# Kernel tuning notes

Hardware: AMD Instinct MI355X
Metric: run time of the kernel (lower is better)

Reference implementation:

```python
import jax, jax.numpy as jnp
import numpy as np

B = 131072
# join branch layer dims: 203 -> 175 -> 150 -> 128 -> 80 -> 48
DIMS = [203, 175, 150, 128, 80, 48]

def setup_inputs() -> dict:
    key = jax.random.key(0)
    ks = jax.random.split(key, 11)
    inp = {"x": jax.random.normal(ks[0], (B, DIMS[0]), dtype=jnp.float32)}
    for i in range(5):
        fan_in, fan_out = DIMS[i], DIMS[i + 1]
        bound = 1.0 / np.sqrt(fan_in)
        inp[f"W{i+1}"] = jax.random.uniform(ks[1 + 2 * i], (fan_out, fan_in), minval=-bound, maxval=bound, dtype=jnp.float32)
        inp[f"b{i+1}"] = jax.random.uniform(ks[2 + 2 * i], (fan_out,), minval=-bound, maxval=bound, dtype=jnp.float32)
    return inp

def reference(x, W1, b1, W2, b2, W3, b3, W4, b4, W5, b5):
    # join branch of NodeEmbedding, dropout in eval mode (identity).
    h = jnp.tanh(x @ W1.T + b1)      # [B,175]
    h = jnp.tanh(h @ W2.T + b2)      # [B,150]
    h = jnp.tanh(h @ W3.T + b3)      # [B,128]
    h = jnp.tanh(h @ W4.T + b4)      # [B,80]
    return h @ W5.T + b5             # [B,48], no activation on last layer
```

## Files before the change

kernel.cpp:

```cpp
#include <hip/hip_runtime.h>


typedef short short8 __attribute__((ext_vector_type(8)));
typedef float f32x16 __attribute__((ext_vector_type(16)));
typedef unsigned int uint;
typedef unsigned short ushort;

#define SROW 196
#define WBHALF 12288


__device__ __forceinline__ ushort f2bf(float f) {
    uint u = __float_as_uint(f);
    u += 0x7FFFu + ((u >> 16) & 1u);
    return (ushort)(u >> 16);
}
__device__ __forceinline__ float bf2f(ushort h) { return __uint_as_float(((uint)h) << 16); }
__device__ __forceinline__ float fast_tanh(float x) {
    float e = __expf(2.0f * x);
    return 1.0f - 2.0f / (e + 1.0f);
}
__device__ __forceinline__ void g2l16(const void* g, void* l) {
    __builtin_amdgcn_global_load_lds((const __attribute__((address_space(1))) uint*)g,
                                     (__attribute__((address_space(3))) uint*)l, 16, 0, 0);
}

union U16x8 { uint u[4]; short8 s; };

__device__ __forceinline__ short8 load_a_lds(const ushort* p) {
    U16x8 r;
    *(uint2*)&r.u[0] = *(const uint2*)(p);
    *(uint2*)&r.u[2] = *(const uint2*)(p + 4);
    return r.s;
}

__global__ void prep_weights(const float* __restrict__ W1, const float* __restrict__ W2,
                             const float* __restrict__ W3, const float* __restrict__ W4,
                             const float* __restrict__ W5, char* __restrict__ ws)
{
    const int b = blockIdx.x, l = threadIdx.x;
    int layer, local;
    if      (b <  78) { layer = 0; local = b; }
    else if (b < 133) { layer = 1; local = b - 78; }
    else if (b < 173) { layer = 2; local = b - 133; }
    else if (b < 197) { layer = 3; local = b - 173; }
    else              { layer = 4; local = b - 197; }
    const int NTa[5]  = {6, 5, 4, 3, 2};
    const int FINa[5] = {203, 175, 150, 128, 80};
    const int FOa[5]  = {175, 150, 128, 80, 48};
    const float* Wp = (layer == 0) ? W1 : (layer == 1) ? W2 : (layer == 2) ? W3
                    : (layer == 3) ? W4 : W5;
    const int nt = NTa[layer], fin = FINa[layer], fout = FOa[layer];
    const int c = local / nt, t = local % nt;
    const int n  = t * 32 + (l & 31);
    const int kb = c * 16 + (l >> 5) * 8;
    uint hw[4], lw[4];
#pragma unroll
    for (int j = 0; j < 8; ++j) {
        int k = kb + j;
        float v = (n < fout && k < fin) ? Wp[(size_t)n * fin + k] : 0.0f;
        ushort hh = f2bf(v);
        ushort ll = f2bf(v - bf2f(hh));
        if (j & 1) { hw[j >> 1] |= ((uint)hh) << 16; lw[j >> 1] |= ((uint)ll) << 16; }
        else       { hw[j >> 1]  = hh;               lw[j >> 1]  = ll; }
    }
    char* dst = ws + (size_t)b * 2048 + l * 16;
    *(uint4*)dst          = make_uint4(hw[0], hw[1], hw[2], hw[3]);
    *(uint4*)(dst + 1024) = make_uint4(lw[0], lw[1], lw[2], lw[3]);
}

template<int KC, int NT, bool ACT, bool LAST, bool FIRST>
__device__ __forceinline__ void run_layer(
    const char* __restrict__ wsL, const float* __restrict__ bias, int FOUT,
    const float* __restrict__ xg,
    const ushort* __restrict__ aHp, const ushort* __restrict__ aLp,
    ushort* __restrict__ oHp, ushort* __restrict__ oLp,
    float* __restrict__ outg,
    char* __restrict__ wbuf, int row0, int tid)
{
    const int l  = tid & 63;
    const int w  = tid >> 6;
    const int rg = w >> 1;
    const int ns = w & 1;
    const int lx = l & 31;
    const int lh = l >> 5;
    constexpr int MT = (NT + 1) / 2;

    f32x16 acc[MT];
#pragma unroll
    for (int m = 0; m < MT; ++m) {
        int t = ns + 2 * m;
        float bv = 0.0f;
        if (t < NT) { int n = t * 32 + lx; bv = (n < FOUT) ? bias[n] : 0.0f; }
#pragma unroll
        for (int r = 0; r < 16; ++r) acc[m][r] = bv;
    }

    __syncthreads();
    for (int idx = w; idx < 2 * NT; idx += 4)
        g2l16(wsL + (size_t)((idx >> 1)) * 2048 + (idx & 1) * 1024 + l * 16,
              wbuf + idx * 1024);

#pragma unroll 1
    for (int c = 0; c < KC; ++c) {
        __syncthreads();
        if (c + 1 < KC) {
            char* dst = wbuf + ((c + 1) & 1) * WBHALF;
            for (int idx = w; idx < 2 * NT; idx += 4)
                g2l16(wsL + (size_t)((c + 1) * NT + (idx >> 1)) * 2048 + (idx & 1) * 1024 + l * 16,
                      dst + idx * 1024);
        }
        short8 aH, aL;
        if (FIRST) {
            float v[8];
#pragma unroll
            for (int j = 0; j < 8; ++j) {
                int k = c * 16 + lh * 8 + j;
                v[j] = (k < 203) ? xg[(size_t)(rg * 32 + lx) * 203 + k] : 0.0f;
            }
            U16x8 h, lo;
#pragma unroll
            for (int j = 0; j < 8; ++j) {
                ushort hh = f2bf(v[j]);
                ushort ll = f2bf(v[j] - bf2f(hh));
                if (j & 1) { h.u[j >> 1] |= ((uint)hh) << 16; lo.u[j >> 1] |= ((uint)ll) << 16; }
                else       { h.u[j >> 1]  = hh;               lo.u[j >> 1]  = ll; }
            }
            aH = h.s; aL = lo.s;
        } else {
            const int off = (rg * 32 + lx) * SROW + c * 16 + lh * 8;
            aH = load_a_lds(aHp + off);
            aL = load_a_lds(aLp + off);
        }
        const char* cb = wbuf + (c & 1) * WBHALF;
#pragma unroll
        for (int m = 0; m < MT; ++m) {
            int t = ns + 2 * m;
            if (t < NT) {
                short8 bH = *(const short8*)(cb + (2 * t) * 1024 + l * 16);
                short8 bL = *(const short8*)(cb + (2 * t + 1) * 1024 + l * 16);
                acc[m] = __builtin_amdgcn_mfma_f32_32x32x16_bf16(aH, bH, acc[m], 0, 0, 0);
                acc[m] = __builtin_amdgcn_mfma_f32_32x32x16_bf16(aL, bH, acc[m], 0, 0, 0);
                acc[m] = __builtin_amdgcn_mfma_f32_32x32x16_bf16(aH, bL, acc[m], 0, 0, 0);
            }
        }
    }
    __syncthreads();

#pragma unroll
    for (int m = 0; m < MT; ++m) {
        int t = ns + 2 * m;
        if (t < NT) {
#pragma unroll
            for (int r = 0; r < 16; ++r) {
                float vv = acc[m][r];
                if (ACT) vv = fast_tanh(vv);
                int rowl = rg * 32 + (r & 3) + 8 * (r >> 2) + 4 * lh;
                int col  = t * 32 + lx;
                if (LAST) {
                    if (col < 48)
                        outg[(size_t)(row0 + rowl) * 48 + col] = vv;
                } else {
                    ushort hh = f2bf(vv);
                    ushort ll = f2bf(vv - bf2f(hh));
                    oHp[rowl * SROW + col] = hh;
                    oLp[rowl * SROW + col] = ll;
                }
            }
        }
    }
}

__global__ __launch_bounds__(256, 2)
void mlp_mfma(const float* __restrict__ x,
              const float* __restrict__ b1, const float* __restrict__ b2,
              const float* __restrict__ b3, const float* __restrict__ b4,
              const float* __restrict__ b5,
              const char* __restrict__ ws, float* __restrict__ out)
{
    __shared__ __align__(16) ushort actH[64 * SROW];
    __shared__ __align__(16) ushort actL[64 * SROW];
    __shared__ __align__(16) char   wbuf[2 * WBHALF];

    const int tid  = threadIdx.x;
    const int row0 = blockIdx.x * 64;
    const float* xg = x + (size_t)row0 * 203;

    run_layer<13, 6, true,  false, true >(ws,              b1, 175, xg,      nullptr, nullptr, actH, actL, nullptr, wbuf, row0, tid);
    run_layer<11, 5, true,  false, false>(ws +  78 * 2048, b2, 150, nullptr, actH, actL, actH, actL, nullptr, wbuf, row0, tid);
    run_layer<10, 4, true,  false, false>(ws + 133 * 2048, b3, 128, nullptr, actH, actL, actH, actL, nullptr, wbuf, row0, tid);
    run_layer< 8, 3, true,  false, false>(ws + 173 * 2048, b4,  80, nullptr, actH, actL, actH, actL, nullptr, wbuf, row0, tid);
    run_layer< 5, 2, false, true,  false>(ws + 197 * 2048, b5,  48, nullptr, actH, actL, actH, actL, out,     wbuf, row0, tid);
}

extern "C" void kernel_launch(void* const* d_in, const int* in_sizes, int n_in,
                              void* d_out, int out_size, void* d_ws, size_t ws_size,
                              hipStream_t stream) {
    (void)in_sizes; (void)n_in; (void)ws_size; (void)out_size;
    const float* x  = (const float*)d_in[0];
    const float* W1 = (const float*)d_in[1];
    const float* b1 = (const float*)d_in[2];
    const float* W2 = (const float*)d_in[3];
    const float* b2 = (const float*)d_in[4];
    const float* W3 = (const float*)d_in[5];
    const float* b3 = (const float*)d_in[6];
    const float* W4 = (const float*)d_in[7];
    const float* b4 = (const float*)d_in[8];
    const float* W5 = (const float*)d_in[9];
    const float* b5 = (const float*)d_in[10];
    float* out = (float*)d_out;
    char* ws = (char*)d_ws;

    hipLaunchKernelGGL(prep_weights, dim3(207), dim3(64), 0, stream,
                       W1, W2, W3, W4, W5, ws);
    hipLaunchKernelGGL(mlp_mfma, dim3(131072 / 64), dim3(256), 0, stream,
                       x, b1, b2, b3, b4, b5, ws, out);
}
```

Before: 344.3 us.

## Read weights directly from global, pack hi/lo activations, stage x coalesced via LDS

```diff
diff --git a/kernel.cpp b/kernel.cpp
--- a/kernel.cpp
+++ b/kernel.cpp
@@ -6,9 +6,8 @@
 typedef unsigned int uint;
 typedef unsigned short ushort;
 
-#define SROW 196
-#define WBHALF 12288
-
+#define SROW 180
+#define XSTR 20
 
 __device__ __forceinline__ ushort f2bf(float f) {
     uint u = __float_as_uint(f);
@@ -20,19 +19,12 @@
     float e = __expf(2.0f * x);
     return 1.0f - 2.0f / (e + 1.0f);
 }
-__device__ __forceinline__ void g2l16(const void* g, void* l) {
-    __builtin_amdgcn_global_load_lds((const __attribute__((address_space(1))) uint*)g,
-                                     (__attribute__((address_space(3))) uint*)l, 16, 0, 0);
-}
-
-union U16x8 { uint u[4]; short8 s; };
-
-__device__ __forceinline__ short8 load_a_lds(const ushort* p) {
-    U16x8 r;
-    *(uint2*)&r.u[0] = *(const uint2*)(p);
-    *(uint2*)&r.u[2] = *(const uint2*)(p + 4);
-    return r.s;
-}
+__device__ __forceinline__ uint rbf(float v) {
+    uint u = __float_as_uint(v);
+    return u + 0x7FFFu + ((u >> 16) & 1u);
+}
+
+union U4S8 { uint4 u; short8 s; };
 
 __global__ void prep_weights(const float* __restrict__ W1, const float* __restrict__ W2,
                              const float* __restrict__ W3, const float* __restrict__ W4,
@@ -69,84 +61,10 @@
     *(uint4*)(dst + 1024) = make_uint4(lw[0], lw[1], lw[2], lw[3]);
 }
 
-template<int KC, int NT, bool ACT, bool LAST, bool FIRST>
-__device__ __forceinline__ void run_layer(
-    const char* __restrict__ wsL, const float* __restrict__ bias, int FOUT,
-    const float* __restrict__ xg,
-    const ushort* __restrict__ aHp, const ushort* __restrict__ aLp,
-    ushort* __restrict__ oHp, ushort* __restrict__ oLp,
-    float* __restrict__ outg,
-    char* __restrict__ wbuf, int row0, int tid)
-{
-    const int l  = tid & 63;
-    const int w  = tid >> 6;
-    const int rg = w >> 1;
-    const int ns = w & 1;
-    const int lx = l & 31;
-    const int lh = l >> 5;
-    constexpr int MT = (NT + 1) / 2;
-
-    f32x16 acc[MT];
-#pragma unroll
-    for (int m = 0; m < MT; ++m) {
-        int t = ns + 2 * m;
-        float bv = 0.0f;
-        if (t < NT) { int n = t * 32 + lx; bv = (n < FOUT) ? bias[n] : 0.0f; }
-#pragma unroll
-        for (int r = 0; r < 16; ++r) acc[m][r] = bv;
-    }
-
-    __syncthreads();
-    for (int idx = w; idx < 2 * NT; idx += 4)
-        g2l16(wsL + (size_t)((idx >> 1)) * 2048 + (idx & 1) * 1024 + l * 16,
-              wbuf + idx * 1024);
-
-#pragma unroll 1
-    for (int c = 0; c < KC; ++c) {
-        __syncthreads();
-        if (c + 1 < KC) {
-            char* dst = wbuf + ((c + 1) & 1) * WBHALF;
-            for (int idx = w; idx < 2 * NT; idx += 4)
-                g2l16(wsL + (size_t)((c + 1) * NT + (idx >> 1)) * 2048 + (idx & 1) * 1024 + l * 16,
-                      dst + idx * 1024);
-        }
-        short8 aH, aL;
-        if (FIRST) {
-            float v[8];
-#pragma unroll
-            for (int j = 0; j < 8; ++j) {
-                int k = c * 16 + lh * 8 + j;
-                v[j] = (k < 203) ? xg[(size_t)(rg * 32 + lx) * 203 + k] : 0.0f;
-            }
-            U16x8 h, lo;
-#pragma unroll
-            for (int j = 0; j < 8; ++j) {
-                ushort hh = f2bf(v[j]);
-                ushort ll = f2bf(v[j] - bf2f(hh));
-                if (j & 1) { h.u[j >> 1] |= ((uint)hh) << 16; lo.u[j >> 1] |= ((uint)ll) << 16; }
-                else       { h.u[j >> 1]  = hh;               lo.u[j >> 1]  = ll; }
-            }
-            aH = h.s; aL = lo.s;
-        } else {
-            const int off = (rg * 32 + lx) * SROW + c * 16 + lh * 8;
-            aH = load_a_lds(aHp + off);
-            aL = load_a_lds(aLp + off);
-        }
-        const char* cb = wbuf + (c & 1) * WBHALF;
-#pragma unroll
-        for (int m = 0; m < MT; ++m) {
-            int t = ns + 2 * m;
-            if (t < NT) {
-                short8 bH = *(const short8*)(cb + (2 * t) * 1024 + l * 16);
-                short8 bL = *(const short8*)(cb + (2 * t + 1) * 1024 + l * 16);
-                acc[m] = __builtin_amdgcn_mfma_f32_32x32x16_bf16(aH, bH, acc[m], 0, 0, 0);
-                acc[m] = __builtin_amdgcn_mfma_f32_32x32x16_bf16(aL, bH, acc[m], 0, 0, 0);
-                acc[m] = __builtin_amdgcn_mfma_f32_32x32x16_bf16(aH, bL, acc[m], 0, 0, 0);
-            }
-        }
-    }
-    __syncthreads();
-
+template<int MT, int NT, int FOUT, int PADN, bool ACT, bool LAST>
+__device__ __forceinline__ void d_phase(f32x16* acc, uint* oP, float* outg,
+                                        int row0, int rg, int ns, int lx, int lh, int tid)
+{
 #pragma unroll
     for (int m = 0; m < MT; ++m) {
         int t = ns + 2 * m;
@@ -158,39 +76,177 @@
                 int rowl = rg * 32 + (r & 3) + 8 * (r >> 2) + 4 * lh;
                 int col  = t * 32 + lx;
                 if (LAST) {
-                    if (col < 48)
-                        outg[(size_t)(row0 + rowl) * 48 + col] = vv;
-                } else {
-                    ushort hh = f2bf(vv);
-                    ushort ll = f2bf(vv - bf2f(hh));
-                    oHp[rowl * SROW + col] = hh;
-                    oLp[rowl * SROW + col] = ll;
+                    if (col < 48) outg[(size_t)(row0 + rowl) * 48 + col] = vv;
+                } else if (col < FOUT) {
+                    uint r1  = rbf(vv);
+                    uint hib = r1 & 0xFFFF0000u;
+                    float lo = vv - __uint_as_float(hib);
+                    uint r2  = rbf(lo);
+                    oP[rowl * SROW + col] = hib | (r2 >> 16);
                 }
             }
         }
     }
-}
-
-__global__ __launch_bounds__(256, 2)
+    if (!LAST) {
+        if (PADN > 0) {
+            for (int idx = tid; idx < 64 * PADN; idx += 256) {
+                int row = idx / PADN, p = idx % PADN;
+                oP[row * SROW + FOUT + p] = 0u;
+            }
+        }
+        __syncthreads();
+    }
+}
+
+template<int KC, int NT, int FOUT, int PADN, bool ACT, bool LAST>
+__device__ __forceinline__ void run_layer(const char* __restrict__ wsL,
+    const float* __restrict__ bias, const uint* aP, uint* oP, float* outg,
+    int row0, int l, int rg, int ns, int lx, int lh, int tid)
+{
+    constexpr int MT = (NT + 1) / 2;
+    f32x16 acc[MT];
+#pragma unroll
+    for (int m = 0; m < MT; ++m) {
+        int t = ns + 2 * m;
+        float bv = 0.0f;
+        if (t < NT) { int n = t * 32 + lx; bv = (n < FOUT) ? bias[n] : 0.0f; }
+#pragma unroll
+        for (int r = 0; r < 16; ++r) acc[m][r] = bv;
+    }
+
+#pragma unroll
+    for (int c = 0; c < KC; ++c) {
+        U4S8 bh[MT], bl[MT];
+#pragma unroll
+        for (int m = 0; m < MT; ++m) {
+            int t = ns + 2 * m;
+            if (t < NT) {
+                const uint4* w = (const uint4*)wsL + (size_t)((c * NT + t) * 2) * 64 + l;
+                bh[m].u = w[0];
+                bl[m].u = w[64];
+            }
+        }
+        const uint* ap = aP + (rg * 32 + lx) * SROW + c * 16 + lh * 8;
+        uint4 d0 = *(const uint4*)ap;
+        uint4 d1 = *(const uint4*)(ap + 4);
+        uint dd[8] = {d0.x, d0.y, d0.z, d0.w, d1.x, d1.y, d1.z, d1.w};
+        U4S8 ah, al;
+        uint* aHu = (uint*)&ah; uint* aLu = (uint*)&al;
+#pragma unroll
+        for (int j = 0; j < 4; ++j) {
+            aHu[j] = (dd[2*j] >> 16)     | (dd[2*j + 1] & 0xFFFF0000u);
+            aLu[j] = (dd[2*j] & 0xFFFFu) | (dd[2*j + 1] << 16);
+        }
+#pragma unroll
+        for (int m = 0; m < MT; ++m) {
+            int t = ns + 2 * m;
+            if (t < NT) {
+                acc[m] = __builtin_amdgcn_mfma_f32_32x32x16_bf16(ah.s, bh[m].s, acc[m], 0, 0, 0);
+                acc[m] = __builtin_amdgcn_mfma_f32_32x32x16_bf16(al.s, bh[m].s, acc[m], 0, 0, 0);
+                acc[m] = __builtin_amdgcn_mfma_f32_32x32x16_bf16(ah.s, bl[m].s, acc[m], 0, 0, 0);
+            }
+        }
+    }
+    if (!LAST) __syncthreads();
+    d_phase<MT, NT, FOUT, PADN, ACT, LAST>(acc, oP, outg, row0, rg, ns, lx, lh, tid);
+}
+
+__device__ __forceinline__ void run_first(const float* __restrict__ x,
+    const char* __restrict__ wsL, const float* __restrict__ bias,
+    uint* oP, float* xst, int row0, int l, int rg, int ns, int lx, int lh, int tid)
+{
+    constexpr int KC = 13, NT = 6, MT = 3;
+    f32x16 acc[MT];
+#pragma unroll
+    for (int m = 0; m < MT; ++m) {
+        int n = (ns + 2 * m) * 32 + lx;
+        float bv = (n < 175) ? bias[n] : 0.0f;
+#pragma unroll
+        for (int r = 0; r < 16; ++r) acc[m][r] = bv;
+    }
+
+#pragma unroll
+    for (int i = 0; i < 4; ++i) {
+        int e = i * 256 + tid, row = e >> 4, kk = e & 15;
+        xst[row * XSTR + kk] = x[(size_t)(row0 + row) * 203 + kk];
+    }
+    __syncthreads();
+
+#pragma unroll
+    for (int c = 0; c < KC; ++c) {
+        U4S8 bh[MT], bl[MT];
+#pragma unroll
+        for (int m = 0; m < MT; ++m) {
+            const uint4* w = (const uint4*)wsL + (size_t)((c * 6 + ns + 2 * m) * 2) * 64 + l;
+            bh[m].u = w[0];
+            bl[m].u = w[64];
+        }
+        float pre[4];
+        if (c < 12) {
+#pragma unroll
+            for (int i = 0; i < 4; ++i) {
+                int e = i * 256 + tid, row = e >> 4, kk = e & 15, k = (c + 1) * 16 + kk;
+                pre[i] = (k < 203) ? x[(size_t)(row0 + row) * 203 + k] : 0.0f;
+            }
+        }
+        const float* apf = xst + (rg * 32 + lx) * XSTR + lh * 8;
+        float4 v0 = *(const float4*)apf;
+        float4 v1 = *(const float4*)(apf + 4);
+        float vv[8] = {v0.x, v0.y, v0.z, v0.w, v1.x, v1.y, v1.z, v1.w};
+        uint rh[8], rl[8];
+#pragma unroll
+        for (int j = 0; j < 8; ++j) {
+            rh[j] = rbf(vv[j]);
+            float lo = vv[j] - __uint_as_float(rh[j] & 0xFFFF0000u);
+            rl[j] = rbf(lo);
+        }
+        U4S8 ah, al;
+        uint* aHu = (uint*)&ah; uint* aLu = (uint*)&al;
+#pragma unroll
+        for (int j = 0; j < 4; ++j) {
+            aHu[j] = (rh[2*j] >> 16) | (rh[2*j + 1] & 0xFFFF0000u);
+            aLu[j] = (rl[2*j] >> 16) | (rl[2*j + 1] & 0xFFFF0000u);
+        }
+#pragma unroll
+        for (int m = 0; m < MT; ++m) {
+            acc[m] = __builtin_amdgcn_mfma_f32_32x32x16_bf16(ah.s, bh[m].s, acc[m], 0, 0, 0);
+            acc[m] = __builtin_amdgcn_mfma_f32_32x32x16_bf16(al.s, bh[m].s, acc[m], 0, 0, 0);
+            acc[m] = __builtin_amdgcn_mfma_f32_32x32x16_bf16(ah.s, bl[m].s, acc[m], 0, 0, 0);
+        }
+        if (c < 12) {
+            __syncthreads();
+#pragma unroll
+            for (int i = 0; i < 4; ++i) {
+                int e = i * 256 + tid, row = e >> 4, kk = e & 15;
+                xst[row * XSTR + kk] = pre[i];
+            }
+            __syncthreads();
+        }
+    }
+    d_phase<MT, NT, 175, 1, true, false>(acc, oP, nullptr, row0, rg, ns, lx, lh, tid);
+}
+
+__global__ __launch_bounds__(256, 3)
 void mlp_mfma(const float* __restrict__ x,
               const float* __restrict__ b1, const float* __restrict__ b2,
               const float* __restrict__ b3, const float* __restrict__ b4,
               const float* __restrict__ b5,
               const char* __restrict__ ws, float* __restrict__ out)
 {
-    __shared__ __align__(16) ushort actH[64 * SROW];
-    __shared__ __align__(16) ushort actL[64 * SROW];
-    __shared__ __align__(16) char   wbuf[2 * WBHALF];
-
-    const int tid  = threadIdx.x;
+    __shared__ __align__(16) uint  actP[64 * SROW];
+    __shared__ __align__(16) float xst[64 * XSTR];
+
+    const int tid = threadIdx.x;
+    const int l = tid & 63, w = tid >> 6;
+    const int rg = w >> 1, ns = w & 1;
+    const int lx = l & 31, lh = l >> 5;
     const int row0 = blockIdx.x * 64;
-    const float* xg = x + (size_t)row0 * 203;
-
-    run_layer<13, 6, true,  false, true >(ws,              b1, 175, xg,      nullptr, nullptr, actH, actL, nullptr, wbuf, row0, tid);
-    run_layer<11, 5, true,  false, false>(ws +  78 * 2048, b2, 150, nullptr, actH, actL, actH, actL, nullptr, wbuf, row0, tid);
-    run_layer<10, 4, true,  false, false>(ws + 133 * 2048, b3, 128, nullptr, actH, actL, actH, actL, nullptr, wbuf, row0, tid);
-    run_layer< 8, 3, true,  false, false>(ws + 173 * 2048, b4,  80, nullptr, actH, actL, actH, actL, nullptr, wbuf, row0, tid);
-    run_layer< 5, 2, false, true,  false>(ws + 197 * 2048, b5,  48, nullptr, actH, actL, actH, actL, out,     wbuf, row0, tid);
+
+    run_first(x, ws, b1, actP, xst, row0, l, rg, ns, lx, lh, tid);
+    run_layer<11, 5, 150, 10, true,  false>(ws +  78 * 2048, b2, actP, actP, nullptr, row0, l, rg, ns, lx, lh, tid);
+    run_layer<10, 4, 128,  0, true,  false>(ws + 133 * 2048, b3, actP, actP, nullptr, row0, l, rg, ns, lx, lh, tid);
+    run_layer< 8, 3,  80,  0, true,  false>(ws + 173 * 2048, b4, actP, actP, nullptr, row0, l, rg, ns, lx, lh, tid);
+    run_layer< 5, 2,  48,  0, false, true >(ws + 197 * 2048, b5, actP, actP, out,     row0, l, rg, ns, lx, lh, tid);
 }
 
 extern "C" void kernel_launch(void* const* d_in, const int* in_sizes, int n_in,
```

Measured after the change: 298.8 us. 1.15x faster.
